# Optimization experiments

Measured on AMD Instinct MI355X. Metric: run time of the kernel, lower is better.

## Reference

```python
import jax, jax.numpy as jnp
import numpy as np

N = 100000   # nodes
E = 600000   # edges
B = 512      # graphs in batch
H = 128      # hidden dim
ED = 8       # edge feature dim
TWO48 = float(2 ** 48 - 1)


def _w(k, shape, fan_in):
    return jax.random.normal(k, shape, jnp.float32) * (1.0 / np.sqrt(fan_in))


def setup_inputs() -> dict:
    key = jax.random.key(0)
    ks = jax.random.split(key, 32)
    inp = {}
    inp["s_node_ids"] = jax.random.randint(ks[0], (N,), 0, 2 ** 31 - 1, dtype=jnp.int32)
    inp["s_edge_index"] = jax.random.randint(ks[1], (2, E), 0, N, dtype=jnp.int32)
    inp["s_edge_attr"] = jax.random.normal(ks[2], (E, ED), jnp.float32)
    inp["s_batch"] = jnp.sort(jax.random.randint(ks[3], (N,), 0, B, dtype=jnp.int32))
    inp["depth"] = jax.random.uniform(ks[4], (B,), jnp.float32)
    # id_mlp: Linear(1,H) -> ReLU -> Linear(H,H)
    inp["id_w1"] = _w(ks[5], (1, H), 1); inp["id_b1"] = jnp.zeros((H,), jnp.float32)
    inp["id_w2"] = _w(ks[6], (H, H), H); inp["id_b2"] = jnp.zeros((H,), jnp.float32)
    # edge_mlp: Linear(ED,H) -> ReLU -> Linear(H,H)
    inp["ed_w1"] = _w(ks[7], (ED, H), ED); inp["ed_b1"] = jnp.zeros((H,), jnp.float32)
    inp["ed_w2"] = _w(ks[8], (H, H), H); inp["ed_b2"] = jnp.zeros((H,), jnp.float32)
    # GINEConv nn MLPs: Linear(H,H) -> ReLU -> Linear(H,H)
    inp["c1_w1"] = _w(ks[9], (H, H), H); inp["c1_b1"] = jnp.zeros((H,), jnp.float32)
    inp["c1_w2"] = _w(ks[10], (H, H), H); inp["c1_b2"] = jnp.zeros((H,), jnp.float32)
    inp["c2_w1"] = _w(ks[11], (H, H), H); inp["c2_b1"] = jnp.zeros((H,), jnp.float32)
    inp["c2_w2"] = _w(ks[12], (H, H), H); inp["c2_b2"] = jnp.zeros((H,), jnp.float32)
    inp["rg_w1"] = _w(ks[13], (H + 1, H), H + 1); inp["rg_b1"] = jnp.zeros((H,), jnp.float32)
    inp["rg_w2"] = _w(ks[14], (H, 1), H); inp["rg_b2"] = jnp.zeros((1,), jnp.float32)
    return inp


def _mlp2(x, w1, b1, w2, b2):
    return jax.nn.relu(x @ w1 + b1) @ w2 + b2


def _gine(x, src, dst, e, w1, b1, w2, b2):
    # message = ReLU(x_j + e), sum-aggregated at dst; out = nn((1+eps)*x + aggr), eps=0
    msg = jax.nn.relu(x[src] + e)                       # [E, H]
    aggr = jax.ops.segment_sum(msg, dst, num_segments=N)  # [N, H]
    return _mlp2(x + aggr, w1, b1, w2, b2)


def _global_mean(x, batch):
    sums = jax.ops.segment_sum(x, batch, num_segments=B)                          # [B, H]
    cnts = jax.ops.segment_sum(jnp.ones((x.shape[0], 1), x.dtype), batch, num_segments=B)
    return sums / jnp.maximum(cnts, 1.0)


def reference(s_node_ids, s_edge_index, s_edge_attr, s_batch, depth,
              id_w1, id_b1, id_w2, id_b2,
              ed_w1, ed_b1, ed_w2, ed_b2,
              c1_w1, c1_b1, c1_w2, c1_b2,
              c2_w1, c2_b1, c2_w2, c2_b2,
              rg_w1, rg_b1, rg_w2, rg_b2):
    src, dst = s_edge_index[0], s_edge_index[1]
    x0 = jnp.clip(s_node_ids.astype(jnp.float32) / TWO48, 0.0, 1.0)[:, None]  # [N,1]
    x = _mlp2(x0, id_w1, id_b1, id_w2, id_b2)                                 # [N,H]
    e = _mlp2(s_edge_attr, ed_w1, ed_b1, ed_w2, ed_b2)                        # [E,H]
    x = jax.nn.relu(_gine(x, src, dst, e, c1_w1, c1_b1, c1_w2, c1_b2))
    x = jax.nn.relu(_gine(x, src, dst, e, c2_w1, c2_b1, c2_w2, c2_b2))
    rep = jnp.concatenate([_global_mean(x, s_batch), depth[:, None]], axis=1)  # [B,H+1]
    return _mlp2(rep, rg_w1, rg_b1, rg_w2, rg_b2)[:, 0]                        # [B]
```

## Files before the change

### kernel.cpp

```cpp
#include <hip/hip_runtime.h>
#include <hip/hip_bf16.h>

#define N_NODES 100000
#define N_EDGES 600000
#define NB      512
#define H       128
#define ED      8
#define SCAN_CHUNK 1024
#define N_CHUNKS   98

typedef __attribute__((ext_vector_type(8))) short short8;
typedef __attribute__((ext_vector_type(4))) float f32x4;
typedef __attribute__((ext_vector_type(4))) unsigned int u32x4;
typedef unsigned short u16;
typedef unsigned int   u32;

static __device__ __forceinline__ u16 f2bf(float f) {
    u32 u = __float_as_uint(f);
    u32 r = u + 0x7fffu + ((u >> 16) & 1u);
    return (u16)(r >> 16);
}
static __device__ __forceinline__ float bf2f(u32 h) {
    return __uint_as_float(h << 16);
}
static __device__ __forceinline__ u32 bfpack(float lo, float hi) {
    u32 r;
    asm("v_cvt_pk_bf16_f32 %0, %1, %2" : "=v"(r) : "v"(lo), "v"(hi));
    return r;
}

__global__ __launch_bounds__(256) void pack_hist_kernel(
    const float* __restrict__ W0, const float* __restrict__ W1,
    const float* __restrict__ W2, const float* __restrict__ W3,
    const float* __restrict__ W4, const float* __restrict__ W5,
    const float* __restrict__ W6,
    short8* __restrict__ O0, short8* __restrict__ O1,
    short8* __restrict__ O2, short8* __restrict__ O3,
    short8* __restrict__ O4, short8* __restrict__ O5,
    short8* __restrict__ O6,
    const int* __restrict__ edge_index, int* __restrict__ counts,
    uint4* __restrict__ sums_zero)
{
    const int HIST_BLKS = (N_EDGES + 255) / 256;
    if (blockIdx.x >= 50 + HIST_BLKS) {
        int idx = (blockIdx.x - 50 - HIST_BLKS) * 256 + threadIdx.x;
        if (idx < 16512) sums_zero[idx] = make_uint4(0, 0, 0, 0);
        return;
    }
    if (blockIdx.x >= 50) {
        int e = (blockIdx.x - 50) * 256 + threadIdx.x;
        if (e < N_EDGES) atomicAdd(&counts[edge_index[N_EDGES + e]], 1);
        return;
    }
    int gid = blockIdx.x * 256 + threadIdx.x;
    const float* W; short8* O; int Krows, kkmax, slot;
    if (gid < 512) { W = W0; O = O0; Krows = ED; kkmax = 1; slot = gid; }
    else {
        int m = (gid - 512) / 2048;
        slot = (gid - 512) % 2048;
        Krows = H; kkmax = 4;
        switch (m) {
            case 0: W = W1; O = O1; break;
            case 1: W = W2; O = O2; break;
            case 2: W = W3; O = O3; break;
            case 3: W = W4; O = O4; break;
            case 4: W = W5; O = O5; break;
            default: W = W6; O = O6; break;
        }
    }
    int lane = slot & 63;
    int t = slot >> 6;
    int nt = t & 1; t >>= 1;
    int kk = t % kkmax;
    int w  = t / kkmax;
    int quad = lane >> 4, n15 = lane & 15;
    int n = w * 32 + nt * 16 + n15;
    short8 v;
    #pragma unroll
    for (int j = 0; j < 8; j++) {
        int k = kk * 32 + quad * 8 + j;
        v[j] = (k < Krows) ? (short)f2bf(W[k * H + n]) : (short)0;
    }
    O[slot] = v;
}

__global__ __launch_bounds__(256) void scan_node_kernel(
    const int* __restrict__ counts, int* __restrict__ chunk_scan,
    int* __restrict__ bsum_raw,
    const int* __restrict__ ids,
    const float* __restrict__ w1, const float* __restrict__ b1,
    const short8* __restrict__ pW2, const float* __restrict__ b2,
    u16* __restrict__ x_out)
{
    __shared__ u16 sH[64 * 136];
    __shared__ float s_x0[64];
    __shared__ int sS[256];
    int tid = threadIdx.x;

    if (blockIdx.x < N_CHUNKS) {
        int base = blockIdx.x * SCAN_CHUNK + tid * 4;
        int4 v = *(const int4*)&counts[base];
        int q0 = v.x, q1 = q0 + v.y, q2 = q1 + v.z, q3 = q2 + v.w;
        sS[tid] = q3;
        __syncthreads();
        #pragma unroll
        for (int off = 1; off < 256; off <<= 1) {
            int t = (tid >= off) ? sS[tid - off] : 0;
            __syncthreads();
            sS[tid] += t;
            __syncthreads();
        }
        int excl = sS[tid] - q3;
        int4 o;
        o.x = excl; o.y = excl + q0; o.z = excl + q1; o.w = excl + q2;
        *(int4*)&chunk_scan[base] = o;
        if (tid == 255) bsum_raw[blockIdx.x] = sS[255];
        return;
    }

    int bid = blockIdx.x - N_CHUNKS;
    int w = tid >> 6, lane = tid & 63, quad = lane >> 4, n15 = lane & 15;
    short8 fW2[4][2];
    #pragma unroll
    for (int kk = 0; kk < 4; kk++) {
        fW2[kk][0] = pW2[((w * 4 + kk) * 2 + 0) * 64 + lane];
        fW2[kk][1] = pW2[((w * 4 + kk) * 2 + 1) * 64 + lane];
    }
    float rb2[2] = { b2[w * 32 + n15], b2[w * 32 + 16 + n15] };
    float w1c = w1[tid & 127], b1c = b1[tid & 127];
    const int ntile = (N_NODES + 63) / 64;
    for (int tile = bid; tile < ntile; tile += 1563) {
        int row0 = tile * 64;
        if (tid < 64) {
            int n = row0 + tid;
            float x0 = (n < N_NODES) ? (float)ids[n] / 281474976710655.0f : 0.0f;
            s_x0[tid] = fminf(fmaxf(x0, 0.0f), 1.0f);
        }
        __syncthreads();
        int half = tid >> 7, c = tid & 127;
        #pragma unroll
        for (int rr = 0; rr < 32; rr += 2) {
            int r = half + rr * 2;
            u32 p = bfpack(fmaxf(s_x0[r] * w1c + b1c, 0.0f),
                           fmaxf(s_x0[r + 2] * w1c + b1c, 0.0f));
            sH[r * 136 + c]       = (u16)p;
            sH[(r + 2) * 136 + c] = (u16)(p >> 16);
        }
        __syncthreads();
        f32x4 acc[4][2];
        #pragma unroll
        for (int s = 0; s < 4; s++) { acc[s][0] = (f32x4){0,0,0,0}; acc[s][1] = (f32x4){0,0,0,0}; }
        #pragma unroll
        for (int kk = 0; kk < 4; kk++) {
            #pragma unroll
            for (int s = 0; s < 4; s++) {
                short8 a = *(const short8*)&sH[(s * 16 + n15) * 136 + kk * 32 + quad * 8];
                acc[s][0] = __builtin_amdgcn_mfma_f32_16x16x32_bf16(a, fW2[kk][0], acc[s][0], 0, 0, 0);
                acc[s][1] = __builtin_amdgcn_mfma_f32_16x16x32_bf16(a, fW2[kk][1], acc[s][1], 0, 0, 0);
            }
        }
        __syncthreads();
        #pragma unroll
        for (int s = 0; s < 4; s++)
            #pragma unroll
            for (int nt = 0; nt < 2; nt++) {
                int col = w * 32 + nt * 16 + n15;
                int rb = (s * 16 + quad * 4) * 136 + col;
                u32 p0 = bfpack(acc[s][nt][0] + rb2[nt], acc[s][nt][1] + rb2[nt]);
                u32 p1 = bfpack(acc[s][nt][2] + rb2[nt], acc[s][nt][3] + rb2[nt]);
                sH[rb]       = (u16)p0;
                sH[rb + 136] = (u16)(p0 >> 16);
                sH[rb + 272] = (u16)p1;
                sH[rb + 408] = (u16)(p1 >> 16);
            }
        __syncthreads();
        for (int idx = tid; idx < 64 * 16; idx += 256) {
            int r = idx >> 4, c8 = (idx & 15) << 3;
            int n = row0 + r;
            if (n < N_NODES)
                *(uint4*)&x_out[(long)n * H + c8] = *(const uint4*)&sH[r * 136 + c8];
        }
        __syncthreads();
    }
}

__global__ __launch_bounds__(256) void fill_kernel(
    const int* __restrict__ edge_index,
    const int* __restrict__ chunk_scan, const int* __restrict__ bsum_raw,
    int* __restrict__ counts, int* __restrict__ src_list,
    const float* __restrict__ attr, u16* __restrict__ attr_perm)
{
    __shared__ int sB[128];
    int tid = threadIdx.x;
    int v0 = 0;
    if (tid < 128) {
        v0 = (tid < N_CHUNKS) ? bsum_raw[tid] : 0;
        sB[tid] = v0;
    }
    __syncthreads();
    #pragma unroll
    for (int off = 1; off < 128; off <<= 1) {
        int t = (tid < 128 && tid >= off) ? sB[tid - off] : 0;
        __syncthreads();
        if (tid < 128) sB[tid] += t;
        __syncthreads();
    }
    if (tid < 128) sB[tid] -= v0;
    __syncthreads();

    int e = blockIdx.x * 256 + tid;
    if (e >= N_EDGES) return;
    int src = edge_index[e];
    int dst = edge_index[N_EDGES + e];
    int slot = atomicAdd(&counts[dst], -1) - 1;
    int pos = chunk_scan[dst] + sB[dst >> 10] + slot;
    src_list[pos] = src;
    float4 a0 = *(const float4*)&attr[(long)e * ED];
    float4 a1 = *(const float4*)&attr[(long)e * ED + 4];
    u32 w0 = bfpack(a0.x, a0.y);
    u32 w1 = bfpack(a0.z, a0.w);
    u32 w2 = bfpack(a1.x, a1.y);
    u32 w3 = bfpack(a1.z, a1.w);
    *(uint4*)&attr_perm[(long)pos * ED] = make_uint4(w0, w1, w2, w3);
}

__global__ __launch_bounds__(256) void edge_mlp_mfma(
    const u16* __restrict__ attr_perm,
    const int* __restrict__ chunk_scan, const int* __restrict__ bsum_raw,
    int* __restrict__ row_start,
    const short8* __restrict__ pW1, const float* __restrict__ b1,
    const short8* __restrict__ pW2, const float* __restrict__ b2,
    u16* __restrict__ e_perm)
{
    __shared__ u16 sH[64 * 136];
    __shared__ int sB[128];
    int tid = threadIdx.x;

    if (blockIdx.x < 392) {
        int v0 = 0;
        if (tid < 128) {
            v0 = (tid < N_CHUNKS) ? bsum_raw[tid] : 0;
            sB[tid] = v0;
        }
        __syncthreads();
        #pragma unroll
        for (int off = 1; off < 128; off <<= 1) {
            int t = (tid < 128 && tid >= off) ? sB[tid - off] : 0;
            __syncthreads();
            if (tid < 128) sB[tid] += t;
            __syncthreads();
        }
        if (tid < 128) sB[tid] -= v0;
        __syncthreads();
        int i = blockIdx.x * 256 + tid;
        if (i <= N_NODES) row_start[i] = chunk_scan[i] + sB[i >> 10];
        __syncthreads();
    }

    int w = tid >> 6, lane = tid & 63, quad = lane >> 4, n15 = lane & 15;
    short8 fW1[2];
    fW1[0] = pW1[(w * 2 + 0) * 64 + lane];
    fW1[1] = pW1[(w * 2 + 1) * 64 + lane];
    short8 fW2[4][2];
    #pragma unroll
    for (int kk = 0; kk < 4; kk++) {
        fW2[kk][0] = pW2[((w * 4 + kk) * 2 + 0) * 64 + lane];
        fW2[kk][1] = pW2[((w * 4 + kk) * 2 + 1) * 64 + lane];
    }
    float rb1[2] = { b1[w * 32 + n15], b1[w * 32 + 16 + n15] };
    float rb2[2] = { b2[w * 32 + n15], b2[w * 32 + 16 + n15] };
    const short8 zero8 = (short8){0,0,0,0,0,0,0,0};
    const int ntile = N_EDGES / 64;
    for (int tile = blockIdx.x; tile < ntile; tile += gridDim.x) {
        int row0 = tile * 64;
        short8 av[4];
        #pragma unroll
        for (int s = 0; s < 4; s++) {
            av[s] = zero8;
            if (quad == 0)
                av[s] = *(const short8*)&attr_perm[(long)(row0 + s * 16 + n15) * ED];
        }
        f32x4 acc[4][2];
        #pragma unroll
        for (int s = 0; s < 4; s++) { acc[s][0] = (f32x4){0,0,0,0}; acc[s][1] = (f32x4){0,0,0,0}; }
        #pragma unroll
        for (int s = 0; s < 4; s++) {
            acc[s][0] = __builtin_amdgcn_mfma_f32_16x16x32_bf16(av[s], fW1[0], acc[s][0], 0, 0, 0);
            acc[s][1] = __builtin_amdgcn_mfma_f32_16x16x32_bf16(av[s], fW1[1], acc[s][1], 0, 0, 0);
        }
        #pragma unroll
        for (int s = 0; s < 4; s++)
            #pragma unroll
            for (int nt = 0; nt < 2; nt++) {
                int col = w * 32 + nt * 16 + n15;
                int rb = (s * 16 + quad * 4) * 136 + col;
                u32 p0 = bfpack(fmaxf(acc[s][nt][0] + rb1[nt], 0.0f),
                                fmaxf(acc[s][nt][1] + rb1[nt], 0.0f));
                u32 p1 = bfpack(fmaxf(acc[s][nt][2] + rb1[nt], 0.0f),
                                fmaxf(acc[s][nt][3] + rb1[nt], 0.0f));
                sH[rb]       = (u16)p0;
                sH[rb + 136] = (u16)(p0 >> 16);
                sH[rb + 272] = (u16)p1;
                sH[rb + 408] = (u16)(p1 >> 16);
            }
        __syncthreads();
        #pragma unroll
        for (int s = 0; s < 4; s++) { acc[s][0] = (f32x4){0,0,0,0}; acc[s][1] = (f32x4){0,0,0,0}; }
        #pragma unroll
        for (int kk = 0; kk < 4; kk++) {
            #pragma unroll
            for (int s = 0; s < 4; s++) {
                short8 a = *(const short8*)&sH[(s * 16 + n15) * 136 + kk * 32 + quad * 8];
                acc[s][0] = __builtin_amdgcn_mfma_f32_16x16x32_bf16(a, fW2[kk][0], acc[s][0], 0, 0, 0);
                acc[s][1] = __builtin_amdgcn_mfma_f32_16x16x32_bf16(a, fW2[kk][1], acc[s][1], 0, 0, 0);
            }
        }
        __syncthreads();
        #pragma unroll
        for (int s = 0; s < 4; s++)
            #pragma unroll
            for (int nt = 0; nt < 2; nt++) {
                int col = w * 32 + nt * 16 + n15;
                int rb = (s * 16 + quad * 4) * 136 + col;
                u32 p0 = bfpack(acc[s][nt][0] + rb2[nt], acc[s][nt][1] + rb2[nt]);
                u32 p1 = bfpack(acc[s][nt][2] + rb2[nt], acc[s][nt][3] + rb2[nt]);
                sH[rb]       = (u16)p0;
                sH[rb + 136] = (u16)(p0 >> 16);
                sH[rb + 272] = (u16)p1;
                sH[rb + 408] = (u16)(p1 >> 16);
            }
        __syncthreads();
        for (int idx = tid; idx < 64 * 16; idx += 256) {
            int r = idx >> 4, c8 = (idx & 15) << 3;
            *(uint4*)&e_perm[(long)(row0 + r) * H + c8] = *(const uint4*)&sH[r * 136 + c8];
        }
        __syncthreads();
    }
}

static __device__ __forceinline__ void acc8(float* a, u32x4 xv, u32x4 ev) {
    #pragma unroll
    for (int q = 0; q < 4; q++) {
        a[2 * q + 0] += fmaxf(bf2f(xv[q] & 0xffff) + bf2f(ev[q] & 0xffff), 0.0f);
        a[2 * q + 1] += fmaxf(bf2f(xv[q] >> 16)    + bf2f(ev[q] >> 16),    0.0f);
    }
}

__global__ __launch_bounds__(256) void gine_fused(
    const int* __restrict__ row_start,
    const int* __restrict__ src_list,
    const u16* __restrict__ e_perm,
    const u16* __restrict__ x,
    const short8* __restrict__ pW1, const float* __restrict__ b1,
    const short8* __restrict__ pW2, const float* __restrict__ b2,
    u16* __restrict__ x_out,
    const int* __restrict__ batch, float* __restrict__ sums,
    float* __restrict__ cnt, int do_pool)
{
    __shared__ u16 sA[16 * 136];
    __shared__ int sBt[16];
    int tid  = threadIdx.x;
    int lane = tid & 63;
    int l16  = lane & 15;
    int base = lane & 48;
    int fo   = l16 * 8;
    int r    = tid >> 4;
    int n    = blockIdx.x * 16 + r;
    const u16* xb = x + fo;

    if (do_pool && tid < 16) sBt[tid] = batch[blockIdx.x * 16 + tid];

    int beg = row_start[n];
    int end = row_start[n + 1];
    float a[8], b[8];
    #pragma unroll
    for (int q = 0; q < 8; q++) { a[q] = 0.0f; b[q] = 0.0f; }

    for (int j0 = beg; j0 < end; j0 += 16) {
        int m = min(16, end - j0);
        int sv = src_list[j0 + min(l16, m - 1)];
        const u16* ej = e_perm + (long)j0 * H + fo;
        int j = 0;
        for (; j + 2 <= m; j += 2) {
            int s0 = __shfl(sv, base | j);
            int s1 = __shfl(sv, base | (j + 1));
            u32x4 xv0 = *(const u32x4*)(xb + (long)s0 * H);
            u32x4 ev0 = *(const u32x4*)(ej + (long)(j + 0) * H);
            u32x4 xv1 = *(const u32x4*)(xb + (long)s1 * H);
            u32x4 ev1 = *(const u32x4*)(ej + (long)(j + 1) * H);
            acc8(a, xv0, ev0);
            acc8(b, xv1, ev1);
        }
        if (j < m) {
            int s0 = __shfl(sv, base | j);
            u32x4 xv0 = *(const u32x4*)(xb + (long)s0 * H);
            u32x4 ev0 = *(const u32x4*)(ej + (long)j * H);
            acc8(a, xv0, ev0);
        }
    }
    u32x4 xself = *(const u32x4*)(xb + (long)n * H);
    u32x4 xsrow;
    #pragma unroll
    for (int q = 0; q < 4; q++) {
        float o0 = bf2f(xself[q] & 0xffff) + a[2 * q + 0] + b[2 * q + 0];
        float o1 = bf2f(xself[q] >> 16)    + a[2 * q + 1] + b[2 * q + 1];
        xsrow[q] = bfpack(o0, o1);
    }
    *(uint4*)&sA[r * 136 + fo] = *(uint4*)&xsrow;
    __syncthreads();

    int w = tid >> 6, quad = lane >> 4, n15 = l16;
    float rb1[2] = { b1[w * 32 + n15], b1[w * 32 + 16 + n15] };
    float rb2[2] = { b2[w * 32 + n15], b2[w * 32 + 16 + n15] };
    f32x4 acc[2];
    acc[0] = (f32x4){0,0,0,0}; acc[1] = (f32x4){0,0,0,0};
    #pragma unroll
    for (int kk = 0; kk < 4; kk++) {
        short8 av = *(const short8*)&sA[n15 * 136 + kk * 32 + quad * 8];
        short8 w0 = pW1[((w * 4 + kk) * 2 + 0) * 64 + lane];
        short8 w1v = pW1[((w * 4 + kk) * 2 + 1) * 64 + lane];
        acc[0] = __builtin_amdgcn_mfma_f32_16x16x32_bf16(av, w0, acc[0], 0, 0, 0);
        acc[1] = __builtin_amdgcn_mfma_f32_16x16x32_bf16(av, w1v, acc[1], 0, 0, 0);
    }
    __syncthreads();
    #pragma unroll
    for (int nt = 0; nt < 2; nt++) {
        int col = w * 32 + nt * 16 + n15;
        int rb = (quad * 4) * 136 + col;
        u32 p0 = bfpack(fmaxf(acc[nt][0] + rb1[nt], 0.0f),
                        fmaxf(acc[nt][1] + rb1[nt], 0.0f));
        u32 p1 = bfpack(fmaxf(acc[nt][2] + rb1[nt], 0.0f),
                        fmaxf(acc[nt][3] + rb1[nt], 0.0f));
        sA[rb]       = (u16)p0;
        sA[rb + 136] = (u16)(p0 >> 16);
        sA[rb + 272] = (u16)p1;
        sA[rb + 408] = (u16)(p1 >> 16);
    }
    __syncthreads();
    acc[0] = (f32x4){0,0,0,0}; acc[1] = (f32x4){0,0,0,0};
    #pragma unroll
    for (int kk = 0; kk < 4; kk++) {
        short8 av = *(const short8*)&sA[n15 * 136 + kk * 32 + quad * 8];
        short8 w0 = pW2[((w * 4 + kk) * 2 + 0) * 64 + lane];
        short8 w1v = pW2[((w * 4 + kk) * 2 + 1) * 64 + lane];
        acc[0] = __builtin_amdgcn_mfma_f32_16x16x32_bf16(av, w0, acc[0], 0, 0, 0);
        acc[1] = __builtin_amdgcn_mfma_f32_16x16x32_bf16(av, w1v, acc[1], 0, 0, 0);
    }
    __syncthreads();
    #pragma unroll
    for (int nt = 0; nt < 2; nt++) {
        int col = w * 32 + nt * 16 + n15;
        int rb = (quad * 4) * 136 + col;
        u32 p0 = bfpack(fmaxf(acc[nt][0] + rb2[nt], 0.0f),
                        fmaxf(acc[nt][1] + rb2[nt], 0.0f));
        u32 p1 = bfpack(fmaxf(acc[nt][2] + rb2[nt], 0.0f),
                        fmaxf(acc[nt][3] + rb2[nt], 0.0f));
        sA[rb]       = (u16)p0;
        sA[rb + 136] = (u16)(p0 >> 16);
        sA[rb + 272] = (u16)p1;
        sA[rb + 408] = (u16)(p1 >> 16);
    }
    __syncthreads();
    if (!do_pool) {
        int rr = tid >> 4, c8 = (tid & 15) << 3;
        int nn = blockIdx.x * 16 + rr;
        *(uint4*)&x_out[(long)nn * H + c8] = *(const uint4*)&sA[rr * 136 + c8];
    } else {
        if (tid < 64) {
            int c2 = tid * 2;
            float s0 = 0.0f, s1 = 0.0f;
            int cur = sBt[0];
            #pragma unroll
            for (int rr = 0; rr < 16; rr++) {
                int bb = sBt[rr];
                if (bb != cur) {
                    atomicAdd(&sums[cur * H + c2],     s0);
                    atomicAdd(&sums[cur * H + c2 + 1], s1);
                    s0 = s1 = 0.0f; cur = bb;
                }
                u32 v = *(const u32*)&sA[rr * 136 + c2];
                s0 += bf2f(v & 0xffff);
                s1 += bf2f(v >> 16);
            }
            atomicAdd(&sums[cur * H + c2],     s0);
            atomicAdd(&sums[cur * H + c2 + 1], s1);
        } else if (tid == 64) {
            int cur = sBt[0];
            float cc = 0.0f;
            #pragma unroll
            for (int rr = 0; rr < 16; rr++) {
                int bb = sBt[rr];
                if (bb != cur) {
                    atomicAdd(&cnt[cur], cc);
                    cc = 0.0f; cur = bb;
                }
                cc += 1.0f;
            }
            atomicAdd(&cnt[cur], cc);
        }
    }
}

__global__ __launch_bounds__(128) void regressor_kernel(
    const float* __restrict__ sums, const float* __restrict__ cnt,
    const float* __restrict__ depth,
    const float* __restrict__ w1, const float* __restrict__ b1,
    const float* __restrict__ w2, const float* __restrict__ b2,
    float* __restrict__ out)
{
    __shared__ float s_mean[H];
    __shared__ float s_red[2];
    int b = blockIdx.x;
    int j = threadIdx.x;
    float c = fmaxf(cnt[b], 1.0f);
    s_mean[j] = sums[b * H + j] / c;
    __syncthreads();
    float h = b1[j];
    #pragma unroll 8
    for (int k = 0; k < H; k++) h += s_mean[k] * w1[k * H + j];
    h += depth[b] * w1[H * H + j];
    h = fmaxf(h, 0.0f);
    float p = h * w2[j];
    #pragma unroll
    for (int off = 32; off >= 1; off >>= 1) p += __shfl_down(p, off, 64);
    if ((j & 63) == 0) s_red[j >> 6] = p;
    __syncthreads();
    if (j == 0) out[b] = s_red[0] + s_red[1] + b2[0];
}

extern "C" void kernel_launch(void* const* d_in, const int* in_sizes, int n_in,
                              void* d_out, int out_size, void* d_ws, size_t ws_size,
                              hipStream_t stream)
{
    const int*   ids   = (const int*)  d_in[0];
    const int*   eidx  = (const int*)  d_in[1];
    const float* eattr = (const float*)d_in[2];
    const int*   batch = (const int*)  d_in[3];
    const float* depth = (const float*)d_in[4];
    const float* id_w1 = (const float*)d_in[5];
    const float* id_b1 = (const float*)d_in[6];
    const float* id_w2 = (const float*)d_in[7];
    const float* id_b2 = (const float*)d_in[8];
    const float* ed_w1 = (const float*)d_in[9];
    const float* ed_b1 = (const float*)d_in[10];
    const float* ed_w2 = (const float*)d_in[11];
    const float* ed_b2 = (const float*)d_in[12];
    const float* c1_w1 = (const float*)d_in[13];
    const float* c1_b1 = (const float*)d_in[14];
    const float* c1_w2 = (const float*)d_in[15];
    const float* c1_b2 = (const float*)d_in[16];
    const float* c2_w1 = (const float*)d_in[17];
    const float* c2_b1 = (const float*)d_in[18];
    const float* c2_w2 = (const float*)d_in[19];
    const float* c2_b2 = (const float*)d_in[20];
    const float* rg_w1 = (const float*)d_in[21];
    const float* rg_b1 = (const float*)d_in[22];
    const float* rg_w2 = (const float*)d_in[23];
    const float* rg_b2 = (const float*)d_in[24];

    char* ws = (char*)d_ws;
    u16*   e_buf    = (u16*)  (ws);
    u16*   x_buf    = (u16*)  (ws + 153600000);
    u16*   xs_buf   = (u16*)  (ws + 179200000);
    float* sums_buf = (float*)(ws + 204800000);
    float* cnt_buf  = (float*)(ws + 205062144);
    int*   counts   = (int*)  (ws + 205064192);
    int*   chunk_sc = (int*)  (ws + 205465600);
    int*   bsum_raw = (int*)  (ws + 205867008);
    int*   src_list = (int*)  (ws + 205868032);
    short8* ed_w1p  = (short8*)(ws + 208268032);
    short8* ed_w2p  = (short8*)(ws + 208276224);
    short8* c1_w1p  = (short8*)(ws + 208308992);
    short8* c1_w2p  = (short8*)(ws + 208341760);
    short8* c2_w1p  = (short8*)(ws + 208374528);
    short8* c2_w2p  = (short8*)(ws + 208407296);
    short8* id_w2p  = (short8*)(ws + 208440064);
    int*   row_start = counts;
    u16*   attr_perm = xs_buf;

    hipMemsetAsync(counts, 0, 401408, stream);

    const int HIST_BLKS = (N_EDGES + 255) / 256;
    pack_hist_kernel<<<50 + HIST_BLKS + 65, 256, 0, stream>>>(
        ed_w1, ed_w2, c1_w1, c1_w2, c2_w1, c2_w2, id_w2,
        ed_w1p, ed_w2p, c1_w1p, c1_w2p, c2_w1p, c2_w2p, id_w2p,
        eidx, counts, (uint4*)sums_buf);

    scan_node_kernel<<<N_CHUNKS + 1563, 256, 0, stream>>>(
        counts, chunk_sc, bsum_raw,
        ids, id_w1, id_b1, id_w2p, id_b2, x_buf);

    fill_kernel<<<(N_EDGES + 255) / 256, 256, 0, stream>>>(
        eidx, chunk_sc, bsum_raw, counts, src_list, eattr, attr_perm);

    edge_mlp_mfma<<<3125, 256, 0, stream>>>(
        attr_perm, chunk_sc, bsum_raw, row_start,
        ed_w1p, ed_b1, ed_w2p, ed_b2, e_buf);

    gine_fused<<<6250, 256, 0, stream>>>(row_start, src_list, e_buf, x_buf,
                                         c1_w1p, c1_b1, c1_w2p, c1_b2, xs_buf,
                                         batch, sums_buf, cnt_buf, 0);
    gine_fused<<<6250, 256, 0, stream>>>(row_start, src_list, e_buf, xs_buf,
                                         c2_w1p, c2_b1, c2_w2p, c2_b2, x_buf,
                                         batch, sums_buf, cnt_buf, 1);

    regressor_kernel<<<NB, 128, 0, stream>>>(sums_buf, cnt_buf, depth,
                                             rg_w1, rg_b1, rg_w2, rg_b2, (float*)d_out);
}
```

Baseline: 360.8 us.

## Replace pooling atomics with per-block partial sums reduced in regressor

In the pooling pass, each block now writes up to four per-segment partial sums and segment ids to scratch buffers instead of issuing float atomics. The regressor binary-searches the sorted batch array for each graph's node range, adds the matching block partials, and derives the node count from that range, so the count atomics are gone. The node-init grid is also halved so each block handles more tiles. In exchange the regressor does more serial reads, and correctness relies on batch being sorted and on reusing x_buf and chunk_sc as scratch.

```diff
diff --git a/kernel.cpp b/kernel.cpp
--- a/kernel.cpp
+++ b/kernel.cpp
@@ -44,7 +44,7 @@
     const int HIST_BLKS = (N_EDGES + 255) / 256;
     if (blockIdx.x >= 50 + HIST_BLKS) {
         int idx = (blockIdx.x - 50 - HIST_BLKS) * 256 + threadIdx.x;
-        if (idx < 16512) sums_zero[idx] = make_uint4(0, 0, 0, 0);
+        if (idx < 16384) sums_zero[idx] = make_uint4(0, 0, 0, 0);
         return;
     }
     if (blockIdx.x >= 50) {
@@ -129,7 +129,7 @@
     float rb2[2] = { b2[w * 32 + n15], b2[w * 32 + 16 + n15] };
     float w1c = w1[tid & 127], b1c = b1[tid & 127];
     const int ntile = (N_NODES + 63) / 64;
-    for (int tile = bid; tile < ntile; tile += 1563) {
+    for (int tile = bid; tile < ntile; tile += 768) {
         int row0 = tile * 64;
         if (tid < 64) {
             int n = row0 + tid;
@@ -354,8 +354,11 @@
     const short8* __restrict__ pW1, const float* __restrict__ b1,
     const short8* __restrict__ pW2, const float* __restrict__ b2,
     u16* __restrict__ x_out,
-    const int* __restrict__ batch, float* __restrict__ sums,
-    float* __restrict__ cnt, int do_pool)
+    const int* __restrict__ batch,
+    float* __restrict__ sums,
+    float* __restrict__ part_sums,
+    int* __restrict__ part_id,
+    int do_pool)
 {
     __shared__ u16 sA[16 * 136];
     __shared__ int sBt[16];
@@ -470,39 +473,55 @@
             int c2 = tid * 2;
             float s0 = 0.0f, s1 = 0.0f;
             int cur = sBt[0];
+            int seg = 0;
             #pragma unroll
             for (int rr = 0; rr < 16; rr++) {
                 int bb = sBt[rr];
                 if (bb != cur) {
-                    atomicAdd(&sums[cur * H + c2],     s0);
-                    atomicAdd(&sums[cur * H + c2 + 1], s1);
-                    s0 = s1 = 0.0f; cur = bb;
+                    if (seg < 4) {
+                        long pb = ((long)blockIdx.x * 4 + seg) * H;
+                        part_sums[pb + c2]     = s0;
+                        part_sums[pb + c2 + 1] = s1;
+                    } else {
+                        atomicAdd(&sums[cur * H + c2],     s0);
+                        atomicAdd(&sums[cur * H + c2 + 1], s1);
+                    }
+                    s0 = s1 = 0.0f; cur = bb; seg++;
                 }
                 u32 v = *(const u32*)&sA[rr * 136 + c2];
                 s0 += bf2f(v & 0xffff);
                 s1 += bf2f(v >> 16);
             }
-            atomicAdd(&sums[cur * H + c2],     s0);
-            atomicAdd(&sums[cur * H + c2 + 1], s1);
+            if (seg < 4) {
+                long pb = ((long)blockIdx.x * 4 + seg) * H;
+                part_sums[pb + c2]     = s0;
+                part_sums[pb + c2 + 1] = s1;
+            } else {
+                atomicAdd(&sums[cur * H + c2],     s0);
+                atomicAdd(&sums[cur * H + c2 + 1], s1);
+            }
         } else if (tid == 64) {
             int cur = sBt[0];
-            float cc = 0.0f;
+            int seg = 0;
             #pragma unroll
             for (int rr = 0; rr < 16; rr++) {
                 int bb = sBt[rr];
                 if (bb != cur) {
-                    atomicAdd(&cnt[cur], cc);
-                    cc = 0.0f; cur = bb;
+                    if (seg < 4) part_id[blockIdx.x * 4 + seg] = cur;
+                    cur = bb; seg++;
                 }
-                cc += 1.0f;
-            }
-            atomicAdd(&cnt[cur], cc);
+            }
+            if (seg < 4) part_id[blockIdx.x * 4 + seg] = cur;
+            for (int s2 = seg + 1; s2 < 4; s2++) part_id[blockIdx.x * 4 + s2] = -1;
         }
     }
 }
 
 __global__ __launch_bounds__(128) void regressor_kernel(
-    const float* __restrict__ sums, const float* __restrict__ cnt,
+    const float* __restrict__ sums,
+    const float* __restrict__ part_sums,
+    const int* __restrict__ part_id,
+    const int* __restrict__ batch,
     const float* __restrict__ depth,
     const float* __restrict__ w1, const float* __restrict__ b1,
     const float* __restrict__ w2, const float* __restrict__ b2,
@@ -512,8 +531,24 @@
     __shared__ float s_red[2];
     int b = blockIdx.x;
     int j = threadIdx.x;
-    float c = fmaxf(cnt[b], 1.0f);
-    s_mean[j] = sums[b * H + j] / c;
+    int lo = 0, hi = N_NODES;
+    while (lo < hi) { int mid = (lo + hi) >> 1; if (batch[mid] < b) lo = mid + 1; else hi = mid; }
+    int n_start = lo;
+    hi = N_NODES;
+    while (lo < hi) { int mid = (lo + hi) >> 1; if (batch[mid] < b + 1) lo = mid + 1; else hi = mid; }
+    int n_end = lo;
+    float acc = sums[b * H + j];
+    if (n_end > n_start) {
+        int blk0 = n_start >> 4, blk1 = (n_end - 1) >> 4;
+        for (int blk = blk0; blk <= blk1; blk++) {
+            #pragma unroll
+            for (int s = 0; s < 4; s++)
+                if (part_id[blk * 4 + s] == b)
+                    acc += part_sums[((long)blk * 4 + s) * H + j];
+        }
+    }
+    float c = fmaxf((float)(n_end - n_start), 1.0f);
+    s_mean[j] = acc / c;
     __syncthreads();
     float h = b1[j];
     #pragma unroll 8
@@ -563,7 +598,6 @@
     u16*   x_buf    = (u16*)  (ws + 153600000);
     u16*   xs_buf   = (u16*)  (ws + 179200000);
     float* sums_buf = (float*)(ws + 204800000);
-    float* cnt_buf  = (float*)(ws + 205062144);
     int*   counts   = (int*)  (ws + 205064192);
     int*   chunk_sc = (int*)  (ws + 205465600);
     int*   bsum_raw = (int*)  (ws + 205867008);
@@ -577,16 +611,18 @@
     short8* id_w2p  = (short8*)(ws + 208440064);
     int*   row_start = counts;
     u16*   attr_perm = xs_buf;
+    float* part_sums = (float*)x_buf;
+    int*   part_id   = chunk_sc;
 
     hipMemsetAsync(counts, 0, 401408, stream);
 
     const int HIST_BLKS = (N_EDGES + 255) / 256;
-    pack_hist_kernel<<<50 + HIST_BLKS + 65, 256, 0, stream>>>(
+    pack_hist_kernel<<<50 + HIST_BLKS + 64, 256, 0, stream>>>(
         ed_w1, ed_w2, c1_w1, c1_w2, c2_w1, c2_w2, id_w2,
         ed_w1p, ed_w2p, c1_w1p, c1_w2p, c2_w1p, c2_w2p, id_w2p,
         eidx, counts, (uint4*)sums_buf);
 
-    scan_node_kernel<<<N_CHUNKS + 1563, 256, 0, stream>>>(
+    scan_node_kernel<<<N_CHUNKS + 768, 256, 0, stream>>>(
         counts, chunk_sc, bsum_raw,
         ids, id_w1, id_b1, id_w2p, id_b2, x_buf);
 
@@ -599,11 +635,12 @@
 
     gine_fused<<<6250, 256, 0, stream>>>(row_start, src_list, e_buf, x_buf,
                                          c1_w1p, c1_b1, c1_w2p, c1_b2, xs_buf,
-                                         batch, sums_buf, cnt_buf, 0);
+                                         batch, sums_buf, part_sums, part_id, 0);
     gine_fused<<<6250, 256, 0, stream>>>(row_start, src_list, e_buf, xs_buf,
                                          c2_w1p, c2_b1, c2_w2p, c2_b2, x_buf,
-                                         batch, sums_buf, cnt_buf, 1);
-
-    regressor_kernel<<<NB, 128, 0, stream>>>(sums_buf, cnt_buf, depth,
-                                             rg_w1, rg_b1, rg_w2, rg_b2, (float*)d_out);
-}
+                                         batch, sums_buf, part_sums, part_id, 1);
+
+    regressor_kernel<<<NB, 128, 0, stream>>>(sums_buf, part_sums, part_id, batch,
+                                             depth, rg_w1, rg_b1, rg_w2, rg_b2,
+                                             (float*)d_out);
+}
```

Result: no change. 356.4 us (-1.2%).
